# Performance work log

Measured on AMD Instinct MI355X. Metric: run time of the kernel, lower is better.

The kernel has to match this reference:

```python
import jax, jax.numpy as jnp
import numpy as np

B = 4096   # batch
I = 1024   # in_features
O = 1024   # out_features
N = 4      # LUT fan-in; table size 2**N = 16


def setup_inputs() -> dict:
    key = jax.random.key(0)
    k1, k2, k3 = jax.random.split(key, 3)
    return {
        "x": jax.random.normal(k1, (B, I), dtype=jnp.float32),
        # learnable mapping logits: (out_features, n, in_features)
        "mapping_logits": jax.random.normal(k2, (O, N, I), dtype=jnp.float32),
        # per-node LUT tables with 2**n corner values each
        "lut_tables": jax.random.normal(k3, (O, 2 ** N), dtype=jnp.float32),
    }


def reference(x, mapping_logits, lut_tables):
    # softmax-weighted input selection: (B,I) x (O,N,I) -> (B,O,N)
    w = jax.nn.softmax(mapping_logits, axis=-1)
    selected = jnp.einsum('bi,oni->bon', x, w)
    # BatchedLUTNodes: squash to [0,1], multilinear interpolation over 2**N corners
    s = jax.nn.sigmoid(selected)                      # (B,O,N)
    cw = jnp.ones(s.shape[:2] + (1,), dtype=s.dtype)  # corner weights, grows to (B,O,2**N)
    for j in range(N):                                # fixed small loop over fan-in
        sj = s[..., j][..., None]                     # (B,O,1)
        cw = jnp.concatenate([cw * (1.0 - sj), cw * sj], axis=-1)
    # weighted sum of per-node table entries -> (B,O)
    return jnp.einsum('boc,oc->bo', cw, lut_tables)
```

## Files before the change

### kernel.cpp

```cpp
#include <hip/hip_runtime.h>

#define B_DIM 4096
#define I_DIM 1024
#define O_DIM 1024
#define ON_DIM 4096
#define TILE_HALFS 4096

typedef _Float16 half8  __attribute__((ext_vector_type(8)));
typedef _Float16 half4_t __attribute__((ext_vector_type(4)));
typedef float    floatx4 __attribute__((ext_vector_type(4)));

__global__ __launch_bounds__(256)
void ltn_stats(const float* __restrict__ logits, float2* __restrict__ stats) {
  const int t = threadIdx.x, lane = t & 63, wv = t >> 6;
  const int row = blockIdx.x * 4 + wv;
  const float4* src = (const float4*)(logits + (size_t)row * I_DIM);
  float4 v[4];
#pragma unroll
  for (int j = 0; j < 4; j++) v[j] = src[j * 64 + lane];
  float m = -1e30f;
#pragma unroll
  for (int j = 0; j < 4; j++)
    m = fmaxf(m, fmaxf(fmaxf(v[j].x, v[j].y), fmaxf(v[j].z, v[j].w)));
#pragma unroll
  for (int off = 1; off < 64; off <<= 1) m = fmaxf(m, __shfl_xor(m, off));
  float s = 0.0f;
#pragma unroll
  for (int j = 0; j < 4; j++) {
    s += __expf(v[j].x - m) + __expf(v[j].y - m)
       + __expf(v[j].z - m) + __expf(v[j].w - m);
  }
#pragma unroll
  for (int off = 1; off < 64; off <<= 1) s += __shfl_xor(s, off);
  if (lane == 0) stats[row] = make_float2(m, 1.0f / s);
}

__global__ __launch_bounds__(256)
void ltn_tile(const float* __restrict__ logits, const float* __restrict__ x,
              const float2* __restrict__ stats,
              _Float16* __restrict__ wt, _Float16* __restrict__ xt) {
  const int t  = threadIdx.x;
  const int nn = t >> 1;
  const int hf = t & 1;
  if (blockIdx.x < 1024) {
    const int nb = blockIdx.x >> 5, kb = blockIdx.x & 31;
    const int row = nb * 128 + nn;
    const float2 st = stats[row];
    const float4* src = (const float4*)(logits + (size_t)row * I_DIM + kb * 32 + hf * 16);
    const float4 a = src[0], b = src[1], c = src[2], d = src[3];
    half8 h0, h1;
    h0[0] = (_Float16)(__expf(a.x - st.x) * st.y);
    h0[1] = (_Float16)(__expf(a.y - st.x) * st.y);
    h0[2] = (_Float16)(__expf(a.z - st.x) * st.y);
    h0[3] = (_Float16)(__expf(a.w - st.x) * st.y);
    h0[4] = (_Float16)(__expf(b.x - st.x) * st.y);
    h0[5] = (_Float16)(__expf(b.y - st.x) * st.y);
    h0[6] = (_Float16)(__expf(b.z - st.x) * st.y);
    h0[7] = (_Float16)(__expf(b.w - st.x) * st.y);
    h1[0] = (_Float16)(__expf(c.x - st.x) * st.y);
    h1[1] = (_Float16)(__expf(c.y - st.x) * st.y);
    h1[2] = (_Float16)(__expf(c.z - st.x) * st.y);
    h1[3] = (_Float16)(__expf(c.w - st.x) * st.y);
    h1[4] = (_Float16)(__expf(d.x - st.x) * st.y);
    h1[5] = (_Float16)(__expf(d.y - st.x) * st.y);
    h1[6] = (_Float16)(__expf(d.z - st.x) * st.y);
    h1[7] = (_Float16)(__expf(d.w - st.x) * st.y);
    _Float16* base = wt + ((size_t)nb * 32 + kb) * TILE_HALFS + (hf * 2) * 1024 + nn * 8;
    *(half8*)base = h0;
    *(half8*)(base + 1024) = h1;
  } else {
    const int bid = blockIdx.x - 1024;
    const int mb = bid >> 5, kt = bid & 31;
    const int row = mb * 128 + nn;
    const float4* src = (const float4*)(x + (size_t)row * I_DIM + kt * 32 + hf * 16);
    const float4 a = src[0], b = src[1], c = src[2], d = src[3];
    half8 h0, h1;
    h0[0] = (_Float16)a.x; h0[1] = (_Float16)a.y; h0[2] = (_Float16)a.z; h0[3] = (_Float16)a.w;
    h0[4] = (_Float16)b.x; h0[5] = (_Float16)b.y; h0[6] = (_Float16)b.z; h0[7] = (_Float16)b.w;
    h1[0] = (_Float16)c.x; h1[1] = (_Float16)c.y; h1[2] = (_Float16)c.z; h1[3] = (_Float16)c.w;
    h1[4] = (_Float16)d.x; h1[5] = (_Float16)d.y; h1[6] = (_Float16)d.z; h1[7] = (_Float16)d.w;
    _Float16* base = xt + ((size_t)mb * 32 + kt) * TILE_HALFS + (hf * 2) * 1024 + nn * 8;
    *(half8*)base = h0;
    *(half8*)(base + 1024) = h1;
  }
}

__global__ __launch_bounds__(512, 2)
void ltn_gemm_lut(const _Float16* __restrict__ xt,
                  const _Float16* __restrict__ wt,
                  const float* __restrict__ lut,
                  float* __restrict__ out) {
  __shared__ _Float16 sm[3 * 16384];

  const int tid  = threadIdx.x;
  const int lane = tid & 63;
  const int wv   = tid >> 6;
  const int wr   = wv >> 1;
  const int wc   = wv & 1;

  const int id  = blockIdx.x;
  const int xcd = id & 7;
  const int li  = id >> 3;
  const int mb  = (xcd & 3) * 4 + (li & 3);
  const int nb  = (xcd >> 2) * 8 + (li >> 2);

  const int fm = lane & 15;
  const int kq = lane >> 4;

  const size_t baseA = (size_t)(mb * 2) * 32 * TILE_HALFS;
  const size_t baseB = (size_t)(nb * 2) * 32 * TILE_HALFS;

  floatx4 acc[4][8];
#pragma unroll
  for (int i = 0; i < 4; i++)
#pragma unroll
    for (int j = 0; j < 8; j++) acc[i][j] = (floatx4)0.0f;

  auto stage = [&](int bufOff , int kt) {
#pragma unroll
    for (int s = 0; s < 4; s++) {
      const int c   = wv * 4 + s;
      const int cc  = c & 15;
      const int tl  = cc >> 3;
      const int sub = cc & 7;
      const _Float16* g;
      int dst;
      if (c < 16) {
        g = xt + baseA + (size_t)(tl * 32 + kt) * TILE_HALFS + sub * 512 + lane * 8;
        dst = bufOff + cc * 512;
      } else {
        g = wt + baseB + (size_t)(tl * 32 + kt) * TILE_HALFS + sub * 512 + lane * 8;
        dst = bufOff + 8192 + cc * 512;
      }
      __builtin_amdgcn_global_load_lds(
          (const __attribute__((address_space(1))) void*)g,
          (__attribute__((address_space(3))) void*)(sm + dst), 16, 0, 0);
    }
  };

  auto compute = [&](int bufOff) {
    half8 af[4], bf[8];
#pragma unroll
    for (int f = 0; f < 4; f++)
      af[f] = *(const half8*)&sm[bufOff + ((wr >> 1) * 4 + kq) * 1024
                                 + ((wr & 1) * 64 + f * 16 + fm) * 8];
#pragma unroll
    for (int g = 0; g < 8; g++)
      bf[g] = *(const half8*)&sm[bufOff + 8192 + (wc * 4 + kq) * 1024
                                 + (g * 16 + fm) * 8];
    __builtin_amdgcn_s_setprio(1);
#pragma unroll
    for (int mt = 0; mt < 4; mt++)
#pragma unroll
      for (int nt = 0; nt < 8; nt++)
        acc[mt][nt] = __builtin_amdgcn_mfma_f32_16x16x32_f16(
            af[mt], bf[nt], acc[mt][nt], 0, 0, 0);
    __builtin_amdgcn_s_setprio(0);
  };

  stage(0, 0);
  stage(16384, 1);
  int o0 = 0, o1 = 16384, o2 = 32768;

  for (int kt = 0; kt < 32; kt++) {
    if (kt < 31) asm volatile("s_waitcnt vmcnt(4)" ::: "memory");
    else         asm volatile("s_waitcnt vmcnt(0)" ::: "memory");
    __builtin_amdgcn_s_barrier();
    __builtin_amdgcn_sched_barrier(0);
    if (kt + 2 < 32) stage(o2, kt + 2);
    compute(o0);
    const int t0 = o0; o0 = o1; o1 = o2; o2 = t0;
  }

#pragma unroll
  for (int nt = 0; nt < 8; nt++) {
    const int o = (nb * 256 + wc * 128 + nt * 16 + fm) >> 2;
    const float4* lt4 = (const float4*)(lut + (size_t)o * 16);
    const float4 L0 = lt4[0], L1 = lt4[1], L2 = lt4[2], L3 = lt4[3];
#pragma unroll
    for (int mt = 0; mt < 4; mt++) {
#pragma unroll
      for (int r = 0; r < 4; r++) {
        const float v  = acc[mt][nt][r];
        const float sv = 1.0f / (1.0f + __expf(-v));
        const float s1 = __shfl_down(sv, 1);
        const float s2 = __shfl_down(sv, 2);
        const float s3 = __shfl_down(sv, 3);
        if ((lane & 3) == 0) {
          const float s0 = sv;
          const float a0 = L0.x + (L2.x - L0.x) * s3;
          const float a1 = L0.y + (L2.y - L0.y) * s3;
          const float a2 = L0.z + (L2.z - L0.z) * s3;
          const float a3 = L0.w + (L2.w - L0.w) * s3;
          const float a4 = L1.x + (L3.x - L1.x) * s3;
          const float a5 = L1.y + (L3.y - L1.y) * s3;
          const float a6 = L1.z + (L3.z - L1.z) * s3;
          const float a7 = L1.w + (L3.w - L1.w) * s3;
          const float b0 = a0 + (a4 - a0) * s2;
          const float b1 = a1 + (a5 - a1) * s2;
          const float b2 = a2 + (a6 - a2) * s2;
          const float b3 = a3 + (a7 - a3) * s2;
          const float c0 = b0 + (b2 - b0) * s1;
          const float c1 = b1 + (b3 - b1) * s1;
          const float res = c0 + (c1 - c0) * s0;
          const int row = mb * 256 + wr * 64 + mt * 16 + (lane >> 4) * 4 + r;
          out[(size_t)row * O_DIM + o] = res;
        }
      }
    }
  }
}

extern "C" void kernel_launch(void* const* d_in, const int* in_sizes, int n_in,
                              void* d_out, int out_size, void* d_ws, size_t ws_size,
                              hipStream_t stream) {
  const float* x      = (const float*)d_in[0];
  const float* logits = (const float*)d_in[1];
  const float* lut    = (const float*)d_in[2];
  float* out          = (float*)d_out;

  _Float16* wt = (_Float16*)d_ws;
  _Float16* xt = (_Float16*)d_ws + (size_t)ON_DIM * I_DIM;
  float2* stats = (float2*)d_out;

  ltn_stats<<<1024, 256, 0, stream>>>(logits, stats);
  ltn_tile<<<2048, 256, 0, stream>>>(logits, x, stats, wt, xt);
  ltn_gemm_lut<<<256, 512, 0, stream>>>(xt, wt, lut, out);
}
```

Baseline: 132.4 us.

## Deepen GEMM LDS pipeline to four stages with split half-tile compute phases

The GEMM main loop moves from a 3-buffer, 2-ahead prefetch to a 4-buffer, 3-ahead prefetch. Each k-step is split into two phases that each load half of the B fragments, issue half of the next-tile global-to-LDS loads, and run half of the MFMAs. The goal is to hide global load latency better and to interleave LDS reads and async copies with MFMA work. In exchange, LDS use grows to 128KB per block, which may conflict with the two-blocks-per-CU launch bound, and the loop now has more barriers per k-step.

```diff
diff --git a/kernel.cpp b/kernel.cpp
--- a/kernel.cpp
+++ b/kernel.cpp
@@ -90,7 +90,7 @@
                   const _Float16* __restrict__ wt,
                   const float* __restrict__ lut,
                   float* __restrict__ out) {
-  __shared__ _Float16 sm[3 * 16384];
+  __shared__ _Float16 sm[4 * 16384];
 
   const int tid  = threadIdx.x;
   const int lane = tid & 63;
@@ -116,9 +116,9 @@
 #pragma unroll
     for (int j = 0; j < 8; j++) acc[i][j] = (floatx4)0.0f;
 
-  auto stage = [&](int bufOff , int kt) {
-#pragma unroll
-    for (int s = 0; s < 4; s++) {
+  auto stage2 = [&](int bufOff , int kt, int sLo) {
+#pragma unroll
+    for (int s = sLo; s < sLo + 2; s++) {
       const int c   = wv * 4 + s;
       const int cc  = c & 15;
       const int tl  = cc >> 3;
@@ -138,38 +138,64 @@
     }
   };
 
-  auto compute = [&](int bufOff) {
-    half8 af[4], bf[8];
+  stage2(0,     0, 0); stage2(0,     0, 2);
+  stage2(16384, 1, 0); stage2(16384, 1, 2);
+  stage2(32768, 2, 0); stage2(32768, 2, 2);
+  asm volatile("s_waitcnt vmcnt(8)" ::: "memory");
+  __builtin_amdgcn_s_barrier();
+
+  half8 af[4], bf[8];
+
+#pragma unroll 1
+  for (int kt = 0; kt < 32; kt++) {
+    const int rb = (kt & 3) * 16384;
+    const int sb = ((kt + 3) & 3) * 16384;
+    const bool doStage = (kt + 3 < 32);
+
 #pragma unroll
     for (int f = 0; f < 4; f++)
-      af[f] = *(const half8*)&sm[bufOff + ((wr >> 1) * 4 + kq) * 1024
+      af[f] = *(const half8*)&sm[rb + (wr >> 1) * 4096 + kq * 1024
                                  + ((wr & 1) * 64 + f * 16 + fm) * 8];
 #pragma unroll
-    for (int g = 0; g < 8; g++)
-      bf[g] = *(const half8*)&sm[bufOff + 8192 + (wc * 4 + kq) * 1024
+    for (int g = 0; g < 4; g++)
+      bf[g] = *(const half8*)&sm[rb + 8192 + wc * 4096 + kq * 1024
                                  + (g * 16 + fm) * 8];
+    if (doStage) stage2(sb, kt + 3, 0);
+    __builtin_amdgcn_sched_barrier(0);
+    __builtin_amdgcn_s_barrier();
+    asm volatile("s_waitcnt lgkmcnt(0)" ::: "memory");
+    __builtin_amdgcn_sched_barrier(0);
     __builtin_amdgcn_s_setprio(1);
 #pragma unroll
     for (int mt = 0; mt < 4; mt++)
 #pragma unroll
-      for (int nt = 0; nt < 8; nt++)
+      for (int nt = 0; nt < 4; nt++)
         acc[mt][nt] = __builtin_amdgcn_mfma_f32_16x16x32_f16(
             af[mt], bf[nt], acc[mt][nt], 0, 0, 0);
     __builtin_amdgcn_s_setprio(0);
-  };
-
-  stage(0, 0);
-  stage(16384, 1);
-  int o0 = 0, o1 = 16384, o2 = 32768;
-
-  for (int kt = 0; kt < 32; kt++) {
-    if (kt < 31) asm volatile("s_waitcnt vmcnt(4)" ::: "memory");
-    else         asm volatile("s_waitcnt vmcnt(0)" ::: "memory");
-    __builtin_amdgcn_s_barrier();
-    __builtin_amdgcn_sched_barrier(0);
-    if (kt + 2 < 32) stage(o2, kt + 2);
-    compute(o0);
-    const int t0 = o0; o0 = o1; o1 = o2; o2 = t0;
+    __builtin_amdgcn_s_barrier();
+
+#pragma unroll
+    for (int g = 4; g < 8; g++)
+      bf[g] = *(const half8*)&sm[rb + 8192 + wc * 4096 + kq * 1024
+                                 + (g * 16 + fm) * 8];
+    if (doStage) stage2(sb, kt + 3, 2);
+    if (kt < 29)       asm volatile("s_waitcnt vmcnt(8)" ::: "memory");
+    else if (kt == 29) asm volatile("s_waitcnt vmcnt(4)" ::: "memory");
+    else if (kt == 30) asm volatile("s_waitcnt vmcnt(0)" ::: "memory");
+    __builtin_amdgcn_sched_barrier(0);
+    __builtin_amdgcn_s_barrier();
+    asm volatile("s_waitcnt lgkmcnt(0)" ::: "memory");
+    __builtin_amdgcn_sched_barrier(0);
+    __builtin_amdgcn_s_setprio(1);
+#pragma unroll
+    for (int mt = 0; mt < 4; mt++)
+#pragma unroll
+      for (int nt = 4; nt < 8; nt++)
+        acc[mt][nt] = __builtin_amdgcn_mfma_f32_16x16x32_f16(
+            af[mt], bf[nt], acc[mt][nt], 0, 0, 0);
+    __builtin_amdgcn_s_setprio(0);
+    __builtin_amdgcn_s_barrier();
   }
 
 #pragma unroll
@@ -225,5 +251,6 @@
 
   ltn_stats<<<1024, 256, 0, stream>>>(logits, stats);
   ltn_tile<<<2048, 256, 0, stream>>>(logits, x, stats, wt, xt);
-  ltn_gemm_lut<<<256, 512, 0, stream>>>(xt, wt, lut, out);
-}
+  dim3 grid(256);
+  ltn_gemm_lut<<<grid, 512, 0, stream>>>(xt, wt, lut, out);
+}
```

New measurement: 136.1 us. 2.8% more time.

## Double K tile depth and switch GEMM to double-buffered LDS pipeline

Applied to the files above, without the earlier changes.

The GEMM main loop now stages two 32-wide K slices per iteration into a 64KB buffer and alternates between two such buffers, replacing the three-buffer rotation. This halves the number of barriers and loop iterations and gives more MFMA work per synchronization. In exchange, prefetch depth drops to one stage and each iteration waits for all outstanding loads, which may expose memory latency.

```diff
diff --git a/kernel.cpp b/kernel.cpp
--- a/kernel.cpp
+++ b/kernel.cpp
@@ -90,7 +90,7 @@
                   const _Float16* __restrict__ wt,
                   const float* __restrict__ lut,
                   float* __restrict__ out) {
-  __shared__ _Float16 sm[3 * 16384];
+  __shared__ _Float16 sm[2 * 32768];
 
   const int tid  = threadIdx.x;
   const int lane = tid & 63;
@@ -118,19 +118,21 @@
 
   auto stage = [&](int bufOff , int kt) {
 #pragma unroll
-    for (int s = 0; s < 4; s++) {
-      const int c   = wv * 4 + s;
-      const int cc  = c & 15;
-      const int tl  = cc >> 3;
-      const int sub = cc & 7;
+    for (int s = 0; s < 8; s++) {
+      const int c = wv * 8 + s;
       const _Float16* g;
       int dst;
-      if (c < 16) {
-        g = xt + baseA + (size_t)(tl * 32 + kt) * TILE_HALFS + sub * 512 + lane * 8;
-        dst = bufOff + cc * 512;
+      if (c < 32) {
+        const int kk = c >> 4, cc = c & 15, tl = cc >> 3, sub = cc & 7;
+        g = xt + baseA + (size_t)(tl * 32 + kt * 2 + kk) * TILE_HALFS
+              + sub * 512 + lane * 8;
+        dst = bufOff + c * 512;
       } else {
-        g = wt + baseB + (size_t)(tl * 32 + kt) * TILE_HALFS + sub * 512 + lane * 8;
-        dst = bufOff + 8192 + cc * 512;
+        const int cb = c - 32;
+        const int kk = cb >> 4, cc = cb & 15, tl = cc >> 3, sub = cc & 7;
+        g = wt + baseB + (size_t)(tl * 32 + kt * 2 + kk) * TILE_HALFS
+              + sub * 512 + lane * 8;
+        dst = bufOff + 16384 + cb * 512;
       }
       __builtin_amdgcn_global_load_lds(
           (const __attribute__((address_space(1))) void*)g,
@@ -139,37 +141,45 @@
   };
 
   auto compute = [&](int bufOff) {
-    half8 af[4], bf[8];
-#pragma unroll
-    for (int f = 0; f < 4; f++)
-      af[f] = *(const half8*)&sm[bufOff + ((wr >> 1) * 4 + kq) * 1024
-                                 + ((wr & 1) * 64 + f * 16 + fm) * 8];
-#pragma unroll
-    for (int g = 0; g < 8; g++)
-      bf[g] = *(const half8*)&sm[bufOff + 8192 + (wc * 4 + kq) * 1024
-                                 + (g * 16 + fm) * 8];
-    __builtin_amdgcn_s_setprio(1);
-#pragma unroll
-    for (int mt = 0; mt < 4; mt++)
-#pragma unroll
-      for (int nt = 0; nt < 8; nt++)
-        acc[mt][nt] = __builtin_amdgcn_mfma_f32_16x16x32_f16(
-            af[mt], bf[nt], acc[mt][nt], 0, 0, 0);
-    __builtin_amdgcn_s_setprio(0);
+#pragma unroll
+    for (int kk = 0; kk < 2; kk++) {
+      half8 af[4], bf[8];
+#pragma unroll
+      for (int f = 0; f < 4; f++)
+        af[f] = *(const half8*)&sm[bufOff + kk * 8192 + (wr >> 1) * 4096
+                                   + kq * 1024
+                                   + ((wr & 1) * 64 + f * 16 + fm) * 8];
+#pragma unroll
+      for (int g = 0; g < 8; g++)
+        bf[g] = *(const half8*)&sm[bufOff + 16384 + kk * 8192 + wc * 4096
+                                   + kq * 1024 + (g * 16 + fm) * 8];
+      __builtin_amdgcn_s_setprio(1);
+#pragma unroll
+      for (int mt = 0; mt < 4; mt++)
+#pragma unroll
+        for (int nt = 0; nt < 8; nt++)
+          acc[mt][nt] = __builtin_amdgcn_mfma_f32_16x16x32_f16(
+              af[mt], bf[nt], acc[mt][nt], 0, 0, 0);
+      __builtin_amdgcn_s_setprio(0);
+    }
   };
 
   stage(0, 0);
-  stage(16384, 1);
-  int o0 = 0, o1 = 16384, o2 = 32768;
-
-  for (int kt = 0; kt < 32; kt++) {
-    if (kt < 31) asm volatile("s_waitcnt vmcnt(4)" ::: "memory");
-    else         asm volatile("s_waitcnt vmcnt(0)" ::: "memory");
-    __builtin_amdgcn_s_barrier();
+  asm volatile("s_waitcnt vmcnt(0)" ::: "memory");
+  __builtin_amdgcn_s_barrier();
+
+  int buf = 0;
+#pragma unroll 1
+  for (int kt = 0; kt < 16; kt++) {
+    const int bo = buf * 32768;
+    if (kt + 1 < 16) stage((buf ^ 1) * 32768, kt + 1);
     __builtin_amdgcn_sched_barrier(0);
-    if (kt + 2 < 32) stage(o2, kt + 2);
-    compute(o0);
-    const int t0 = o0; o0 = o1; o1 = o2; o2 = t0;
+    compute(bo);
+    if (kt + 1 < 16) {
+      asm volatile("s_waitcnt vmcnt(0)" ::: "memory");
+      __builtin_amdgcn_s_barrier();
+    }
+    buf ^= 1;
   }
 
 #pragma unroll
```

Measured after the change: 136.6 us. +3.2%, slower.

## Fuse softmax stats and weight tiling into one prep kernel via LDS transpose

Applied to the files above, without the earlier changes.

Merges the separate softmax-statistics kernel and the tiling/conversion kernel into a single prep kernel. Each wave computes a full softmax row in registers, writes fp16 results to shared memory, and the block then re-emits them in the tiled layout. This removes one launch and the second read of the logits. It also adds an unroll-1 pragma on the GEMM main loop, which may change code size and scheduling.

```diff
diff --git a/kernel.cpp b/kernel.cpp
--- a/kernel.cpp
+++ b/kernel.cpp
@@ -11,65 +11,58 @@
 typedef float    floatx4 __attribute__((ext_vector_type(4)));
 
 __global__ __launch_bounds__(256)
-void ltn_stats(const float* __restrict__ logits, float2* __restrict__ stats) {
-  const int t = threadIdx.x, lane = t & 63, wv = t >> 6;
-  const int row = blockIdx.x * 4 + wv;
-  const float4* src = (const float4*)(logits + (size_t)row * I_DIM);
-  float4 v[4];
-#pragma unroll
-  for (int j = 0; j < 4; j++) v[j] = src[j * 64 + lane];
-  float m = -1e30f;
-#pragma unroll
-  for (int j = 0; j < 4; j++)
-    m = fmaxf(m, fmaxf(fmaxf(v[j].x, v[j].y), fmaxf(v[j].z, v[j].w)));
-#pragma unroll
-  for (int off = 1; off < 64; off <<= 1) m = fmaxf(m, __shfl_xor(m, off));
-  float s = 0.0f;
-#pragma unroll
-  for (int j = 0; j < 4; j++) {
-    s += __expf(v[j].x - m) + __expf(v[j].y - m)
-       + __expf(v[j].z - m) + __expf(v[j].w - m);
-  }
-#pragma unroll
-  for (int off = 1; off < 64; off <<= 1) s += __shfl_xor(s, off);
-  if (lane == 0) stats[row] = make_float2(m, 1.0f / s);
-}
-
-__global__ __launch_bounds__(256)
-void ltn_tile(const float* __restrict__ logits, const float* __restrict__ x,
-              const float2* __restrict__ stats,
+void ltn_prep(const float* __restrict__ logits, const float* __restrict__ x,
               _Float16* __restrict__ wt, _Float16* __restrict__ xt) {
-  const int t  = threadIdx.x;
-  const int nn = t >> 1;
-  const int hf = t & 1;
+  const int t = threadIdx.x;
   if (blockIdx.x < 1024) {
-    const int nb = blockIdx.x >> 5, kb = blockIdx.x & 31;
-    const int row = nb * 128 + nn;
-    const float2 st = stats[row];
-    const float4* src = (const float4*)(logits + (size_t)row * I_DIM + kb * 32 + hf * 16);
-    const float4 a = src[0], b = src[1], c = src[2], d = src[3];
-    half8 h0, h1;
-    h0[0] = (_Float16)(__expf(a.x - st.x) * st.y);
-    h0[1] = (_Float16)(__expf(a.y - st.x) * st.y);
-    h0[2] = (_Float16)(__expf(a.z - st.x) * st.y);
-    h0[3] = (_Float16)(__expf(a.w - st.x) * st.y);
-    h0[4] = (_Float16)(__expf(b.x - st.x) * st.y);
-    h0[5] = (_Float16)(__expf(b.y - st.x) * st.y);
-    h0[6] = (_Float16)(__expf(b.z - st.x) * st.y);
-    h0[7] = (_Float16)(__expf(b.w - st.x) * st.y);
-    h1[0] = (_Float16)(__expf(c.x - st.x) * st.y);
-    h1[1] = (_Float16)(__expf(c.y - st.x) * st.y);
-    h1[2] = (_Float16)(__expf(c.z - st.x) * st.y);
-    h1[3] = (_Float16)(__expf(c.w - st.x) * st.y);
-    h1[4] = (_Float16)(__expf(d.x - st.x) * st.y);
-    h1[5] = (_Float16)(__expf(d.y - st.x) * st.y);
-    h1[6] = (_Float16)(__expf(d.z - st.x) * st.y);
-    h1[7] = (_Float16)(__expf(d.w - st.x) * st.y);
-    _Float16* base = wt + ((size_t)nb * 32 + kb) * TILE_HALFS + (hf * 2) * 1024 + nn * 8;
-    *(half8*)base = h0;
-    *(half8*)(base + 1024) = h1;
+    __shared__ _Float16 lbuf[4][1040];
+    const int lane = t & 63, wv = t >> 6;
+    const int row  = blockIdx.x * 4 + wv;
+    const int nb   = row >> 7;
+    const int nnB  = (blockIdx.x * 4) & 127;
+    const float4* s4 = (const float4*)(logits + (size_t)row * I_DIM);
+    float4 v[4];
+#pragma unroll
+    for (int j = 0; j < 4; j++) v[j] = s4[lane * 4 + j];
+    float m = -1e30f;
+#pragma unroll
+    for (int j = 0; j < 4; j++)
+      m = fmaxf(m, fmaxf(fmaxf(v[j].x, v[j].y), fmaxf(v[j].z, v[j].w)));
+#pragma unroll
+    for (int off = 1; off < 64; off <<= 1) m = fmaxf(m, __shfl_xor(m, off));
+    float s = 0.0f;
+#pragma unroll
+    for (int j = 0; j < 4; j++) {
+      v[j].x = __expf(v[j].x - m); v[j].y = __expf(v[j].y - m);
+      v[j].z = __expf(v[j].z - m); v[j].w = __expf(v[j].w - m);
+      s += v[j].x + v[j].y + v[j].z + v[j].w;
+    }
+#pragma unroll
+    for (int off = 1; off < 64; off <<= 1) s += __shfl_xor(s, off);
+    const float inv = 1.0f / s;
+#pragma unroll
+    for (int j = 0; j < 4; j++) {
+      half4_t h;
+      h[0] = (_Float16)(v[j].x * inv); h[1] = (_Float16)(v[j].y * inv);
+      h[2] = (_Float16)(v[j].z * inv); h[3] = (_Float16)(v[j].w * inv);
+      *(half4_t*)&lbuf[wv][lane * 16 + j * 4] = h;
+    }
+    __syncthreads();
+#pragma unroll
+    for (int p = 0; p < 2; p++) {
+      const int u   = t + p * 256;
+      const int nn4 = u & 3;
+      const int kb8 = (u >> 2) & 3;
+      const int kb  = u >> 4;
+      const half8 h = *(const half8*)&lbuf[nn4][kb * 32 + kb8 * 8];
+      _Float16* dst = wt + ((size_t)nb * 32 + kb) * TILE_HALFS
+                    + kb8 * 1024 + (nnB + nn4) * 8;
+      *(half8*)dst = h;
+    }
   } else {
     const int bid = blockIdx.x - 1024;
+    const int nn = t >> 1;
+    const int hf = t & 1;
     const int mb = bid >> 5, kt = bid & 31;
     const int row = mb * 128 + nn;
     const float4* src = (const float4*)(x + (size_t)row * I_DIM + kt * 32 + hf * 16);
@@ -162,6 +155,7 @@
   stage(16384, 1);
   int o0 = 0, o1 = 16384, o2 = 32768;
 
+#pragma unroll 1
   for (int kt = 0; kt < 32; kt++) {
     if (kt < 31) asm volatile("s_waitcnt vmcnt(4)" ::: "memory");
     else         asm volatile("s_waitcnt vmcnt(0)" ::: "memory");
@@ -221,9 +215,7 @@
 
   _Float16* wt = (_Float16*)d_ws;
   _Float16* xt = (_Float16*)d_ws + (size_t)ON_DIM * I_DIM;
-  float2* stats = (float2*)d_out;
-
-  ltn_stats<<<1024, 256, 0, stream>>>(logits, stats);
-  ltn_tile<<<2048, 256, 0, stream>>>(logits, x, stats, wt, xt);
+
+  ltn_prep<<<2048, 256, 0, stream>>>(logits, x, wt, xt);
   ltn_gemm_lut<<<256, 512, 0, stream>>>(xt, wt, lut, out);
 }
```

Measured after the change: 132.8 us. Within noise of the previous version (+0.3%).
